# Optimization experiments

Hardware: AMD Instinct MI355X
Metric: run time of the kernel (lower is better)

## Reference

```python
import jax, jax.numpy as jnp
import numpy as np

# Config mirrors init_kwargs
D_IN, D_OUT, HEADS, SEQ, BATCH = 1024, 64, 16, 2048, 2


def setup_inputs() -> dict:
    key = jax.random.key(0)
    kx, kq, kk, kv = jax.random.split(key, 4)
    scale = 1.0 / np.sqrt(D_IN)
    x = jax.random.normal(kx, (BATCH, SEQ, D_IN), dtype=jnp.float32)
    # Stacked per-head projection weights, [H, d_in, d_out] (qkv_bias=False)
    Wq = jax.random.normal(kq, (HEADS, D_IN, D_OUT), dtype=jnp.float32) * scale
    Wk = jax.random.normal(kk, (HEADS, D_IN, D_OUT), dtype=jnp.float32) * scale
    Wv = jax.random.normal(kv, (HEADS, D_IN, D_OUT), dtype=jnp.float32) * scale
    return {"x": x, "Wq": Wq, "Wk": Wk, "Wv": Wv}


def reference(x, Wq, Wk, Wv):
    # x: [B, S, d_in]; W*: [H, d_in, d_out]
    q = jnp.einsum("bsd,hde->bhse", x, Wq)
    k = jnp.einsum("bsd,hde->bhse", x, Wk)
    v = jnp.einsum("bsd,hde->bhse", x, Wv)
    scores = jnp.einsum("bhse,bhte->bhst", q, k) / jnp.sqrt(
        jnp.asarray(D_OUT, dtype=q.dtype)
    )
    S = x.shape[1]
    causal = jnp.tril(jnp.ones((S, S), dtype=bool))  # [S, S]
    scores = jnp.where(causal[None, None], scores, -jnp.inf)
    attn = jax.nn.softmax(scores, axis=-1)  # dropout=0.0 (eval)
    ctx = jnp.einsum("bhst,bhte->bhse", attn, v)  # [B, H, S, d_out]
    # concat heads on last dim -> [B, S, H*d_out]
    B, H, S2, E = ctx.shape
    return jnp.transpose(ctx, (0, 2, 1, 3)).reshape(B, S2, H * E)
```

## Files before the change

### kernel.cpp

```cpp
#include <hip/hip_runtime.h>
#include <hip/hip_bf16.h>
#include <math.h>

#define BATCH 2
#define SEQ   2048
#define DIN   1024
#define HEADS 16
#define EDIM  64

#define NX   (BATCH*SEQ*DIN)
#define NW   (3*HEADS*DIN*EDIM)
#define NQKV (BATCH*HEADS*SEQ*EDIM)

#define QSCALE 0.18033688011112042f

typedef __attribute__((ext_vector_type(8))) short short8;
typedef __attribute__((ext_vector_type(4))) float f32x4;

static __device__ __forceinline__ ushort f2bf(float f) {
    __hip_bfloat16 h = __float2bfloat16(f);
    return *reinterpret_cast<ushort*>(&h);
}

static __device__ __forceinline__ void gload16(const void* g, void* l) {
    void* gv = const_cast<void*>(g);
    __builtin_amdgcn_global_load_lds(
        (__attribute__((address_space(1))) void*)gv,
        (__attribute__((address_space(3))) void*)l,
        16, 0, 0);
}

static __device__ __forceinline__ void barrier_fenced() {
    asm volatile("" ::: "memory");
    __builtin_amdgcn_s_barrier();
    asm volatile("" ::: "memory");
}

__global__ __launch_bounds__(256) void prep(
    const float* __restrict__ x, const float* __restrict__ Wq,
    const float* __restrict__ Wk, const float* __restrict__ Wv,
    ushort* __restrict__ xb, ushort* __restrict__ wt)
{
    const int t = threadIdx.x;
    if (blockIdx.x < 1024) {
        const int v0 = blockIdx.x * 256 + t;
#pragma unroll
        for (int i = 0; i < 4; ++i) {
            int i4 = (v0 + i * 262144) * 4;
            float4 f = *(const float4*)(x + i4);
            ushort4 o;
            o.x = f2bf(f.x); o.y = f2bf(f.y); o.z = f2bf(f.z); o.w = f2bf(f.w);
            *(ushort4*)(xb + i4) = o;
        }
    } else {
        const int bid = blockIdx.x - 1024;
        const int dt  = bid & 15;
        const int h   = (bid >> 4) & 15;
        const int mat = bid >> 8;

        const float* W = (mat == 0) ? Wq : (mat == 1) ? Wk : Wv;
        const float* src = W + ((size_t)h * DIN + dt * 64) * EDIM;
        ushort* dst = wt + ((size_t)(mat * HEADS + h) * EDIM) * DIN + dt * 64;

        __shared__ ushort T[64][68];
#pragma unroll
        for (int i = 0; i < 16; ++i) {
            int v = t + i * 256;
            int d = v >> 6, e = v & 63;
            T[d][e] = f2bf(src[(size_t)d * EDIM + e]);
        }
        __syncthreads();
#pragma unroll
        for (int i = 0; i < 4; ++i) {
            int v = t + i * 256;
            int e = v >> 4, d4 = (v & 15) << 2;
            ushort4 ov;
            ov.x = T[d4 + 0][e]; ov.y = T[d4 + 1][e];
            ov.z = T[d4 + 2][e]; ov.w = T[d4 + 3][e];
            *(ushort4*)&dst[(size_t)e * DIN + d4] = ov;
        }
    }
}

__global__ __launch_bounds__(256) void qkv_gemm(
    const ushort* __restrict__ xb, const ushort* __restrict__ wt,
    ushort* __restrict__ qkv)
{
    const int bid = blockIdx.x;
    const int xcd = bid & 7;
    const int idx = bid >> 3;
    const int mt  = (xcd >> 1) * 8 + idx / 12;
    const int nt  = (xcd & 1) * 12 + idx % 12;
    const int m0 = mt * 128, n0 = nt * 128;
    const int b  = mt >> 4;

    __shared__ ushort As[2][128][64];
    __shared__ ushort Bs[2][128][64];

    const int t    = threadIdx.x;
    const int lane = t & 63;
    const int w    = t >> 6;
    const int wr   = w >> 1, wc = w & 1;
    const int fr   = lane & 15;
    const int fk   = (lane >> 4) * 8;
    const int rg   = (lane >> 4) * 4;
    const int sw   = (fr & 7) << 3;

    const ushort* xbase = xb + (size_t)m0 * DIN;
    const ushort* wbase = wt + (size_t)n0 * DIN;

    const int lrow = lane >> 3;
    const int lcol = ((lane & 7) ^ (lane >> 3)) << 3;

#define STAGE(buf, k0)                                                          \
    {                                                                           \
        _Pragma("unroll")                                                       \
        for (int j = 0; j < 4; ++j) {                                           \
            const int c = w * 4 + j;                                            \
            gload16(&xbase[(size_t)(c * 8 + lrow) * DIN + (k0) + lcol], &As[buf][c * 8][0]); \
            gload16(&wbase[(size_t)(c * 8 + lrow) * DIN + (k0) + lcol], &Bs[buf][c * 8][0]); \
        }                                                                       \
    }

    f32x4 acc[4][4];
#pragma unroll
    for (int i = 0; i < 4; ++i)
#pragma unroll
        for (int j = 0; j < 4; ++j) acc[i][j] = (f32x4)0.f;

    STAGE(0, 0);
    STAGE(1, 64);

    short8 a[4][2], bfr[4][2];

#define LOAD_FRAGS(cur)                                                         \
    {                                                                           \
        _Pragma("unroll")                                                       \
        for (int rb = 0; rb < 4; ++rb)                                          \
            _Pragma("unroll")                                                   \
            for (int kk = 0; kk < 2; ++kk) {                                    \
                a[rb][kk]   = *(const short8*)&As[cur][wr * 64 + rb * 16 + fr][(kk * 32 + fk) ^ sw]; \
                bfr[rb][kk] = *(const short8*)&Bs[cur][wc * 64 + rb * 16 + fr][(kk * 32 + fk) ^ sw]; \
            }                                                                   \
    }

#define DO_MFMA()                                                               \
    {                                                                           \
        _Pragma("unroll")                                                       \
        for (int kk = 0; kk < 2; ++kk)                                          \
            _Pragma("unroll")                                                   \
            for (int rb = 0; rb < 4; ++rb)                                      \
                _Pragma("unroll")                                               \
                for (int cf = 0; cf < 4; ++cf)                                  \
                    acc[rb][cf] = __builtin_amdgcn_mfma_f32_16x16x32_bf16(a[rb][kk], bfr[cf][kk], acc[rb][cf], 0, 0, 0); \
    }

    for (int kt = 0; kt < 15; ++kt) {
        const int cur = kt & 1;

        asm volatile("s_waitcnt vmcnt(8)" ::: "memory");
        __builtin_amdgcn_sched_barrier(0);
        barrier_fenced();

        LOAD_FRAGS(cur);

        asm volatile("s_waitcnt lgkmcnt(0)" ::: "memory");
        __builtin_amdgcn_sched_barrier(0);
        barrier_fenced();

        if (kt <= 13) STAGE(cur, (kt + 2) * 64);

        DO_MFMA();
    }
    {
        asm volatile("s_waitcnt vmcnt(0)" ::: "memory");
        __builtin_amdgcn_sched_barrier(0);
        barrier_fenced();
        LOAD_FRAGS(1);
        DO_MFMA();
    }
#undef STAGE
#undef LOAD_FRAGS
#undef DO_MFMA

    const int hg  = nt * 2 + wc;
    const int mat = hg >> 4;
    const int h   = hg & 15;
    const int s0  = (m0 & 2047) + wr * 64;
    if (mat < 2) {
        const float sc = (mat == 0) ? QSCALE : 1.0f;
        ushort* dst = qkv + (size_t)mat * NQKV
                    + ((size_t)((b * HEADS + h) * SEQ) + s0) * EDIM;
#pragma unroll
        for (int rb = 0; rb < 4; ++rb)
#pragma unroll
            for (int cf = 0; cf < 4; ++cf)
#pragma unroll
                for (int i = 0; i < 4; ++i)
                    dst[(size_t)(rb * 16 + rg + i) * EDIM + cf * 16 + fr] = f2bf(acc[rb][cf][i] * sc);
    } else {
        ushort* vtb = qkv + (size_t)2 * NQKV + ((size_t)(b * HEADS + h) * EDIM) * SEQ;
#pragma unroll
        for (int rb = 0; rb < 4; ++rb)
#pragma unroll
            for (int cf = 0; cf < 4; ++cf) {
                ushort4 ov;
                ov.x = f2bf(acc[rb][cf][0]); ov.y = f2bf(acc[rb][cf][1]);
                ov.z = f2bf(acc[rb][cf][2]); ov.w = f2bf(acc[rb][cf][3]);
                *(ushort4*)&vtb[(size_t)(cf * 16 + fr) * SEQ + s0 + rb * 16 + rg] = ov;
            }
    }
}

__global__ __launch_bounds__(512) void flash_mfma(
    const ushort* __restrict__ q, const ushort* __restrict__ k,
    const ushort* __restrict__ vt, float* __restrict__ out)
{
    const int bid = blockIdx.x;
    const int it  = 15 - (bid >> 5);
    const int bh  = bid & 31;
    const int b   = bh >> 4;
    const int h   = bh & 15;
    const int KT  = 2 * it + 2;

    const ushort* Qb  = q  + ((size_t)((b * HEADS + h) * SEQ) + it * 128) * EDIM;
    const ushort* Kb  = k  + ((size_t)((b * HEADS + h) * SEQ)) * EDIM;
    const ushort* Vtb = vt + ((size_t)((b * HEADS + h) * EDIM)) * SEQ;

    __shared__ ushort Ks_[2][64][72];
    __shared__ ushort Vs_[2][64][72];
    __shared__ ushort Ps_[8][16][72];

    const int t    = threadIdx.x;
    const int lane = t & 63;
    const int w    = t >> 6;
    const int fr   = lane & 15;
    const int fk   = (lane >> 4) * 8;
    const int rg   = (lane >> 4) * 4;

    const int srow = t >> 3;
    const int scol = (t & 7) * 8;

    const int wrow0 = it * 128 + w * 16;
    const int lastT = wrow0 >> 6;
    const int qrow  = wrow0 + fr;

    short8 qf[2];
#pragma unroll
    for (int kk = 0; kk < 2; ++kk)
        qf[kk] = *(const short8*)&Qb[(size_t)(w * 16 + fr) * EDIM + kk * 32 + fk];

    f32x4 o_[4];
#pragma unroll
    for (int cf = 0; cf < 4; ++cf) o_[cf] = (f32x4)0.f;
    float lpart = 0.f;

    uint4 krv = *(const uint4*)&Kb[(size_t)srow * EDIM + scol];
    uint4 vrv = *(const uint4*)&Vtb[(size_t)srow * SEQ + scol];
    *(uint4*)&Ks_[0][srow][scol] = krv;
    *(uint4*)&Vs_[0][srow][scol] = vrv;
    __syncthreads();

    for (int kt = 0; kt < KT; ++kt) {
        const int cur = kt & 1;

        if (kt + 1 < KT) {
            krv = *(const uint4*)&Kb[(size_t)((kt + 1) * 64 + srow) * EDIM + scol];
            vrv = *(const uint4*)&Vtb[(size_t)srow * SEQ + (kt + 1) * 64 + scol];
        }

        if (kt <= lastT) {
            f32x4 s[4];
#pragma unroll
            for (int cf = 0; cf < 4; ++cf) s[cf] = (f32x4)0.f;
#pragma unroll
            for (int cf = 0; cf < 4; ++cf)
#pragma unroll
                for (int kk = 0; kk < 2; ++kk) {
                    short8 kf = *(const short8*)&Ks_[cur][cf * 16 + fr][kk * 32 + fk];
                    s[cf] = __builtin_amdgcn_mfma_f32_16x16x32_bf16(kf, qf[kk], s[cf], 0, 0, 0);
                }

            const bool dm = (kt == lastT);
            if (dm) {
#pragma unroll
                for (int cf = 0; cf < 4; ++cf)
#pragma unroll
                    for (int i = 0; i < 4; ++i) {
                        int kpos = kt * 64 + cf * 16 + rg + i;
                        if (kpos > qrow) s[cf][i] = -1e30f;
                    }
            }

            float ls = 0.f;
#pragma unroll
            for (int cf = 0; cf < 4; ++cf) {
                float p0 = __builtin_amdgcn_exp2f(s[cf][0]);
                float p1 = __builtin_amdgcn_exp2f(s[cf][1]);
                float p2 = __builtin_amdgcn_exp2f(s[cf][2]);
                float p3 = __builtin_amdgcn_exp2f(s[cf][3]);
                ls += (p0 + p1) + (p2 + p3);
                uint2 pk;
                pk.x = (uint)f2bf(p0) | ((uint)f2bf(p1) << 16);
                pk.y = (uint)f2bf(p2) | ((uint)f2bf(p3) << 16);
                *(uint2*)&Ps_[w][fr][cf * 16 + rg] = pk;
            }
            lpart += ls;

            short8 pf[2];
#pragma unroll
            for (int kb = 0; kb < 2; ++kb)
                pf[kb] = *(const short8*)&Ps_[w][fr][kb * 32 + fk];
#pragma unroll
            for (int cf = 0; cf < 4; ++cf)
#pragma unroll
                for (int kb = 0; kb < 2; ++kb) {
                    short8 vf = *(const short8*)&Vs_[cur][cf * 16 + fr][kb * 32 + fk];
                    o_[cf] = __builtin_amdgcn_mfma_f32_16x16x32_bf16(vf, pf[kb], o_[cf], 0, 0, 0);
                }
        }

        if (kt + 1 < KT) {
            const int nxt = cur ^ 1;
            *(uint4*)&Ks_[nxt][srow][scol] = krv;
            *(uint4*)&Vs_[nxt][srow][scol] = vrv;
            __syncthreads();
        }
    }

    float ls = lpart;
    ls += __shfl_xor(ls, 16);
    ls += __shfl_xor(ls, 32);
    const float inv = 1.f / ls;

    float* rowp = out + ((size_t)(b * SEQ + qrow)) * (HEADS * EDIM) + h * EDIM;
#pragma unroll
    for (int cf = 0; cf < 4; ++cf) {
        f32x4 ov = o_[cf] * inv;
        *(f32x4*)&rowp[cf * 16 + rg] = ov;
    }
}

extern "C" void kernel_launch(void* const* d_in, const int* in_sizes, int n_in,
                              void* d_out, int out_size, void* d_ws, size_t ws_size,
                              hipStream_t stream) {
    const float* x  = (const float*)d_in[0];
    const float* Wq = (const float*)d_in[1];
    const float* Wk = (const float*)d_in[2];
    const float* Wv = (const float*)d_in[3];
    float* out = (float*)d_out;

    ushort* xb  = (ushort*)d_ws;
    ushort* wt  = xb + NX;
    ushort* qkv = wt + NW;

    prep<<<1792, 256, 0, stream>>>(x, Wq, Wk, Wv, xb, wt);
    qkv_gemm<<<768, 256, 0, stream>>>(xb, wt, qkv);
    flash_mfma<<<BATCH * HEADS * (SEQ / 128), 512, 0, stream>>>(
        qkv, qkv + NQKV, qkv + (size_t)2 * NQKV, out);
}
```

Baseline: 85.28 us.

## Stage K/V tiles via direct global-to-LDS loads with XOR swizzle

Replaces the register-staged K/V tile copy in the flash attention kernel with direct global-to-LDS loads (gload16), prefetching two tiles ahead with explicit vmcnt waits and fenced barriers. The LDS layout drops padding to 64 columns and uses an XOR swizzle on the column index to avoid bank conflicts. The aim is to cut VGPR staging traffic and hide load latency. The cost is an extra barrier per iteration and fragile manual waitcnt accounting.

New measurement: 84.41 us. No clear change (-1.0%).

```diff
diff --git a/kernel.cpp b/kernel.cpp
--- a/kernel.cpp
+++ b/kernel.cpp
@@ -227,8 +227,8 @@
     const ushort* Kb  = k  + ((size_t)((b * HEADS + h) * SEQ)) * EDIM;
     const ushort* Vtb = vt + ((size_t)((b * HEADS + h) * EDIM)) * SEQ;
 
-    __shared__ ushort Ks_[2][64][72];
-    __shared__ ushort Vs_[2][64][72];
+    __shared__ ushort Ks_[2][64][64];
+    __shared__ ushort Vs_[2][64][64];
     __shared__ ushort Ps_[8][16][72];
 
     const int t    = threadIdx.x;
@@ -237,9 +237,18 @@
     const int fr   = lane & 15;
     const int fk   = (lane >> 4) * 8;
     const int rg   = (lane >> 4) * 4;
-
-    const int srow = t >> 3;
-    const int scol = (t & 7) * 8;
+    const int sw   = (fr & 7) << 3;
+
+    const int srow8 = lane >> 3;
+    const int sunit = (lane & 7) ^ srow8;
+
+#define FSTAGE(buf, tile)                                                      \
+    {                                                                          \
+        gload16(&Kb[(size_t)((tile) * 64 + w * 8 + srow8) * EDIM + sunit * 8], \
+                &Ks_[buf][w * 8][0]);                                          \
+        gload16(&Vtb[(size_t)(w * 8 + srow8) * SEQ + (tile) * 64 + sunit * 8], \
+                &Vs_[buf][w * 8][0]);                                          \
+    }
 
     const int wrow0 = it * 128 + w * 16;
     const int lastT = wrow0 >> 6;
@@ -249,25 +258,24 @@
 #pragma unroll
     for (int kk = 0; kk < 2; ++kk)
         qf[kk] = *(const short8*)&Qb[(size_t)(w * 16 + fr) * EDIM + kk * 32 + fk];
+    asm volatile("s_waitcnt vmcnt(0)" ::: "memory");
+    __builtin_amdgcn_sched_barrier(0);
 
     f32x4 o_[4];
 #pragma unroll
     for (int cf = 0; cf < 4; ++cf) o_[cf] = (f32x4)0.f;
     float lpart = 0.f;
 
-    uint4 krv = *(const uint4*)&Kb[(size_t)srow * EDIM + scol];
-    uint4 vrv = *(const uint4*)&Vtb[(size_t)srow * SEQ + scol];
-    *(uint4*)&Ks_[0][srow][scol] = krv;
-    *(uint4*)&Vs_[0][srow][scol] = vrv;
-    __syncthreads();
+    FSTAGE(0, 0);
+    FSTAGE(1, 1);
 
     for (int kt = 0; kt < KT; ++kt) {
         const int cur = kt & 1;
 
-        if (kt + 1 < KT) {
-            krv = *(const uint4*)&Kb[(size_t)((kt + 1) * 64 + srow) * EDIM + scol];
-            vrv = *(const uint4*)&Vtb[(size_t)srow * SEQ + (kt + 1) * 64 + scol];
-        }
+        if (kt + 1 < KT) asm volatile("s_waitcnt vmcnt(2)" ::: "memory");
+        else             asm volatile("s_waitcnt vmcnt(0)" ::: "memory");
+        __builtin_amdgcn_sched_barrier(0);
+        barrier_fenced();
 
         if (kt <= lastT) {
             f32x4 s[4];
@@ -277,12 +285,11 @@
             for (int cf = 0; cf < 4; ++cf)
 #pragma unroll
                 for (int kk = 0; kk < 2; ++kk) {
-                    short8 kf = *(const short8*)&Ks_[cur][cf * 16 + fr][kk * 32 + fk];
+                    short8 kf = *(const short8*)&Ks_[cur][cf * 16 + fr][(kk * 32 + fk) ^ sw];
                     s[cf] = __builtin_amdgcn_mfma_f32_16x16x32_bf16(kf, qf[kk], s[cf], 0, 0, 0);
                 }
 
-            const bool dm = (kt == lastT);
-            if (dm) {
+            if (kt == lastT) {
 #pragma unroll
                 for (int cf = 0; cf < 4; ++cf)
 #pragma unroll
@@ -315,18 +322,18 @@
             for (int cf = 0; cf < 4; ++cf)
 #pragma unroll
                 for (int kb = 0; kb < 2; ++kb) {
-                    short8 vf = *(const short8*)&Vs_[cur][cf * 16 + fr][kb * 32 + fk];
+                    short8 vf = *(const short8*)&Vs_[cur][cf * 16 + fr][(kb * 32 + fk) ^ sw];
                     o_[cf] = __builtin_amdgcn_mfma_f32_16x16x32_bf16(vf, pf[kb], o_[cf], 0, 0, 0);
                 }
         }
 
-        if (kt + 1 < KT) {
-            const int nxt = cur ^ 1;
-            *(uint4*)&Ks_[nxt][srow][scol] = krv;
-            *(uint4*)&Vs_[nxt][srow][scol] = vrv;
-            __syncthreads();
-        }
-    }
+        asm volatile("s_waitcnt lgkmcnt(0)" ::: "memory");
+        __builtin_amdgcn_sched_barrier(0);
+        barrier_fenced();
+
+        if (kt + 2 < KT) FSTAGE(cur, kt + 2);
+    }
+#undef FSTAGE
 
     float ls = lpart;
     ls += __shfl_xor(ls, 16);
```
